# Performance work log

Measured on AMD Instinct MI355X. Metric: run time of the kernel, lower is better.

## Reference

```python
import jax, jax.numpy as jnp
import numpy as np

DIM = 384
HEADS = 8


def setup_inputs() -> dict:
    key = jax.random.key(0)
    k_x, k_qkv, k_pw, k_pb = jax.random.split(key, 4)
    x = jax.random.normal(k_x, (8, DIM, 32, 32), dtype=jnp.float32)
    # Conv2d 1x1 weights stored as [out, in]
    w_qkv = jax.random.normal(k_qkv, (3 * DIM, DIM), dtype=jnp.float32) * (DIM ** -0.5)
    w_proj = jax.random.normal(k_pw, (DIM, DIM), dtype=jnp.float32) * (DIM ** -0.5)
    b_proj = jax.random.normal(k_pb, (DIM,), dtype=jnp.float32) * 0.02
    return {"x": x, "w_qkv": w_qkv, "w_proj": w_proj, "b_proj": b_proj}


def reference(x, w_qkv, w_proj, b_proj):
    B, C, H, W = x.shape
    h = HEADS
    d = C // h
    scale = d ** -0.5
    # 1x1 conv == channel-wise linear: [B,3C,H,W]
    qkv = jnp.einsum('oc,bchw->bohw', w_qkv, x)
    q, k, v = jnp.split(qkv, 3, axis=1)
    # B (h d) H W -> B h (H W) d
    def to_heads(y):
        return y.reshape(B, h, d, H * W).transpose(0, 1, 3, 2)
    q, k, v = to_heads(q), to_heads(k), to_heads(v)
    att = jnp.einsum('bhxd,bhyd->bhxy', q * scale, k)
    att = jax.nn.softmax(att, axis=-1)
    out = jnp.einsum('bhxy,bhyd->bhxd', att, v)
    # B h (H W) d -> B (h d) H W
    out = out.transpose(0, 1, 3, 2).reshape(B, C, H, W)
    out = jnp.einsum('oc,bchw->bohw', w_proj, out) + b_proj[None, :, None, None]
    return out
```

## Files before the change

kernel.cpp:

```cpp
#include <hip/hip_runtime.h>
#include <math.h>

typedef unsigned short u16;
typedef __attribute__((ext_vector_type(8))) short short8;
typedef __attribute__((ext_vector_type(8))) unsigned short ushort8;
typedef __attribute__((ext_vector_type(4))) float floatx4;
typedef __attribute__((ext_vector_type(2))) unsigned int uint2v;

#define SEQ 1024
#define CDIM 384
#define NH 8
#define DH 48
#define DP 64
#define NB 8

__device__ __forceinline__ u16 f2bf(float f){
  unsigned int u; __builtin_memcpy(&u, &f, 4);
  u = (u + 0x7fffu + ((u >> 16) & 1u)) >> 16;
  return (u16)u;
}
__device__ __forceinline__ unsigned packbf(float a, float b){
  unsigned ua, ub; __builtin_memcpy(&ua, &a, 4); __builtin_memcpy(&ub, &b, 4);
  ua += 0x7fffu + ((ua >> 16) & 1u);
  ub += 0x7fffu + ((ub >> 16) & 1u);
  return __builtin_amdgcn_perm(ub, ua, 0x07060302);
}
__device__ __forceinline__ void async16(const u16* g, u16* l){
  __builtin_amdgcn_global_load_lds((const __attribute__((address_space(1))) void*)g,
                                   (__attribute__((address_space(3))) void*)l, 16, 0, 0);
}

__global__ __launch_bounds__(256) void prep_kernel(const float* __restrict__ x,
                                                   const float* __restrict__ wq,
                                                   const float* __restrict__ wp,
                                                   u16* __restrict__ xT,
                                                   u16* __restrict__ wdst){
  __shared__ u16 ldsT[64 * 72];
  const int id = blockIdx.x;
  const int t = threadIdx.x;
  if (id < 768){
    const int bx = id & 15, by = (id >> 4) % 6, bz = id / 96;
    const int c0 = by * 64;
    const int s0 = bx * 64;
    const int rr = t >> 2, q4 = t & 3;

    const float* src = x + ((size_t)(bz * CDIM + c0 + rr)) * SEQ + s0;
#pragma unroll
    for (int i = 0; i < 4; i++){
      const int cc = q4 + i * 4;
      float4 f = *(const float4*)(src + cc * 4);
      ldsT[(cc * 4 + 0) * 72 + rr] = f2bf(f.x);
      ldsT[(cc * 4 + 1) * 72 + rr] = f2bf(f.y);
      ldsT[(cc * 4 + 2) * 72 + rr] = f2bf(f.z);
      ldsT[(cc * 4 + 3) * 72 + rr] = f2bf(f.w);
    }
    __syncthreads();
    u16* dst = xT + ((size_t)(bz * SEQ + s0 + rr)) * CDIM + c0 + q4 * 16;
    *(ushort8*)(dst)     = *(const ushort8*)&ldsT[rr * 72 + q4 * 16];
    *(ushort8*)(dst + 8) = *(const ushort8*)&ldsT[rr * 72 + q4 * 16 + 8];
  } else {
    const int NWQ = 3 * CDIM * CDIM;
    const int i = ((id - 768) * 256 + t) * 4;
    const float* src = (i < NWQ) ? (wq + i) : (wp + (i - NWQ));
    float4 f = *(const float4*)src;
    uint2v v; v[0] = packbf(f.x, f.y); v[1] = packbf(f.z, f.w);
    *(uint2v*)(wdst + i) = v;
  }
}

__global__ __launch_bounds__(256) void qkv_kernel(const u16* __restrict__ W,
                                                  const u16* __restrict__ xT,
                                                  u16* __restrict__ qws,
                                                  u16* __restrict__ kws,
                                                  u16* __restrict__ vws){
  __shared__ u16 ldsA[128 * 64];
  __shared__ u16 ldsB[64 * 64];
  const int t = threadIdx.x;
  const int w = t >> 6, l = t & 63;
  const int quad = l >> 4, li = l & 15;
  const int n0 = blockIdx.x * 64;
  const int m0 = blockIdx.y * 128;
  const int b  = blockIdx.z;

  floatx4 acc[2][4];
#pragma unroll
  for (int i = 0; i < 2; i++)
#pragma unroll
    for (int j = 0; j < 4; j++) acc[i][j] = (floatx4)0.0f;

  const u16* xb = xT + (size_t)b * SEQ * CDIM;
  const int swz = li & 7;

  for (int kk = 0; kk < CDIM; kk += 64){
    __syncthreads();
#pragma unroll
    for (int rep = 0; rep < 4; rep++){
      const int cs = rep * 256 + t;
      const int row = cs >> 3, c4 = cs & 7;
      async16(&W[(size_t)(m0 + row) * CDIM + kk + ((c4 ^ (row & 7)) << 3)], &ldsA[cs * 8]);
    }
#pragma unroll
    for (int rep = 0; rep < 2; rep++){
      const int cs = rep * 256 + t;
      const int row = cs >> 3, c4 = cs & 7;
      async16(&xb[(size_t)(n0 + row) * CDIM + kk + ((c4 ^ (row & 7)) << 3)], &ldsB[cs * 8]);
    }
    __syncthreads();
#pragma unroll
    for (int kc = 0; kc < 2; kc++){
      const int rc = ((kc * 4 + quad) ^ swz) << 3;
      short8 af[2], bf[4];
#pragma unroll
      for (int i = 0; i < 2; i++)
        af[i] = *(const short8*)&ldsA[(w * 32 + i * 16 + li) * 64 + rc];
#pragma unroll
      for (int j = 0; j < 4; j++)
        bf[j] = *(const short8*)&ldsB[(j * 16 + li) * 64 + rc];
#pragma unroll
      for (int i = 0; i < 2; i++)
#pragma unroll
        for (int j = 0; j < 4; j++)
          acc[i][j] = __builtin_amdgcn_mfma_f32_16x16x32_bf16(af[i], bf[j], acc[i][j], 0, 0, 0);
    }
  }

  const float qs = 0.14433756729740643f * 1.4426950408889634f;
  const uint2v z2 = (uint2v)0u;
#pragma unroll
  for (int i = 0; i < 2; i++){
    const int obase = m0 + w * 32 + i * 16 + quad * 4;
    const int which = obase / CDIM;
    const int rem = obase - which * CDIM;
    const int h = rem / DH;
    const int dd = rem - h * DH;
    const int pair = b * NH + h;
#pragma unroll
    for (int j = 0; j < 4; j++){
      const int s = n0 + j * 16 + li;
      floatx4 v = acc[i][j];
      if (which == 0){
        uint2v pk; pk[0] = packbf(v[0] * qs, v[1] * qs); pk[1] = packbf(v[2] * qs, v[3] * qs);
        *(uint2v*)&qws[((size_t)pair * SEQ + s) * DP + dd] = pk;
        if ((dd & 48) == 32)
          *(uint2v*)&qws[((size_t)pair * SEQ + s) * DP + dd + 16] = z2;
      } else if (which == 1){
        uint2v pk; pk[0] = packbf(v[0], v[1]); pk[1] = packbf(v[2], v[3]);
        *(uint2v*)&kws[((size_t)pair * SEQ + s) * DP + dd] = pk;
        if ((dd & 48) == 32)
          *(uint2v*)&kws[((size_t)pair * SEQ + s) * DP + dd + 16] = z2;
      } else {
#pragma unroll
        for (int r = 0; r < 4; r++)
          vws[((size_t)pair * DH + dd + r) * SEQ + s] = f2bf(v[r]);
      }
    }
  }
}

__global__ __launch_bounds__(256) void attn_kernel(const u16* __restrict__ qws,
                                                   const u16* __restrict__ kws,
                                                   const u16* __restrict__ vws,
                                                   u16* __restrict__ aT){
  __shared__ u16 ldsK[2][64 * 64];
  __shared__ u16 ldsV[2][48 * 64];
  __shared__ u16 ldsP[64 * 72];

  const int t = threadIdx.x;
  const int w = t >> 6, l = t & 63;
  const int quad = l >> 4, li = l & 15;
  const int id = blockIdx.x;
  const int pair = id & 63;
  const int qb = id >> 6;
  const int b = pair >> 3, h = pair & 7;
  const int qbase = qb * 64 + w * 16;
  const int swz = li & 7;

  const u16* qrow = qws + ((size_t)pair * SEQ + qbase + li) * DP;
  const short8 qf0 = *(const short8*)(qrow + quad * 8);
  const short8 qf1 = *(const short8*)(qrow + 32 + quad * 8);

  floatx4 ot[3];
#pragma unroll
  for (int dt = 0; dt < 3; dt++) ot[dt] = (floatx4)0.0f;
  float m_run = -3.0e38f, l_run = 0.0f;

  const u16* kbase = kws + (size_t)pair * SEQ * DP;
  const u16* vbase = vws + (size_t)pair * DH * SEQ;

  auto stage = [&](int kv, int pp){
#pragma unroll
    for (int rep = 0; rep < 4; rep++){
      const int cs = rep * 256 + t;
      if (cs < 512){
        const int row = cs >> 3, c4 = cs & 7;
        async16(&kbase[(size_t)(kv + row) * DP + ((c4 ^ (row & 7)) << 3)],
                &ldsK[pp][cs * 8]);
      } else if (cs < 896){
        const int cs2 = cs - 512;
        const int row = cs2 >> 3, c4 = cs2 & 7;
        async16(&vbase[(size_t)row * SEQ + kv + ((c4 ^ (row & 7)) << 3)],
                &ldsV[pp][cs2 * 8]);
      }
    }
  };

  u16* prow = ldsP + (w * 16 + li) * 72;

  stage(0, 0);
  for (int i = 0; i < 16; i++){
    const int p = i & 1;
    __syncthreads();
    if (i < 15) stage((i + 1) * 64, p ^ 1);

    floatx4 st[4];
#pragma unroll
    for (int yt = 0; yt < 4; yt++){
      const u16* krow = ldsK[p] + (yt * 16 + li) * 64;
      const short8 kf0 = *(const short8*)(krow + (((0 + quad) ^ swz) << 3));
      const short8 kf1 = *(const short8*)(krow + (((4 + quad) ^ swz) << 3));
      floatx4 z = (floatx4)0.0f;
      z = __builtin_amdgcn_mfma_f32_16x16x32_bf16(kf0, qf0, z, 0, 0, 0);
      z = __builtin_amdgcn_mfma_f32_16x16x32_bf16(kf1, qf1, z, 0, 0, 0);
      st[yt] = z;
    }

    float mx = -3.0e38f;
#pragma unroll
    for (int yt = 0; yt < 4; yt++)
#pragma unroll
      for (int r = 0; r < 4; r++) mx = fmaxf(mx, st[yt][r]);
    mx = fmaxf(mx, __shfl_xor(mx, 16, 64));
    mx = fmaxf(mx, __shfl_xor(mx, 32, 64));
    const float mnew = fmaxf(m_run, mx);
    const float alpha = __builtin_amdgcn_exp2f(m_run - mnew);
    m_run = mnew;

    float ls = 0.0f;
#pragma unroll
    for (int yt = 0; yt < 4; yt++){
      float p0 = __builtin_amdgcn_exp2f(st[yt][0] - mnew);
      float p1 = __builtin_amdgcn_exp2f(st[yt][1] - mnew);
      float p2 = __builtin_amdgcn_exp2f(st[yt][2] - mnew);
      float p3 = __builtin_amdgcn_exp2f(st[yt][3] - mnew);
      ls += (p0 + p1) + (p2 + p3);
      uint2v pk; pk[0] = packbf(p0, p1); pk[1] = packbf(p2, p3);
      *(uint2v*)&prow[yt * 16 + quad * 4] = pk;
    }
    l_run = l_run * alpha + ls;
#pragma unroll
    for (int dt = 0; dt < 3; dt++) ot[dt] *= alpha;

#pragma unroll
    for (int ks = 0; ks < 64; ks += 32){
      const short8 pb = *(const short8*)&ldsP[(w * 16 + li) * 72 + ks + quad * 8];
#pragma unroll
      for (int dt = 0; dt < 3; dt++){
        const short8 vf = *(const short8*)&ldsV[p][(dt * 16 + li) * 64 +
                                                  ((((ks >> 3) + quad) ^ swz) << 3)];
        ot[dt] = __builtin_amdgcn_mfma_f32_16x16x32_bf16(vf, pb, ot[dt], 0, 0, 0);
      }
    }
  }

  float ls = l_run;
  ls += __shfl_xor(ls, 16, 64);
  ls += __shfl_xor(ls, 32, 64);
  const float rl = __builtin_amdgcn_rcpf(ls);
  const int q = qbase + li;
#pragma unroll
  for (int dt = 0; dt < 3; dt++){
    floatx4 v = ot[dt];
    uint2v pk; pk[0] = packbf(v[0] * rl, v[1] * rl); pk[1] = packbf(v[2] * rl, v[3] * rl);
    *(uint2v*)&aT[((size_t)b * SEQ + q) * CDIM + h * DH + dt * 16 + quad * 4] = pk;
  }
}

__global__ __launch_bounds__(256) void proj_kernel(const u16* __restrict__ W,
                                                   const u16* __restrict__ aT,
                                                   const float* __restrict__ bias,
                                                   float* __restrict__ out){
  __shared__ u16 ldsA[128 * 64];
  __shared__ u16 ldsB[64 * 64];
  const int t = threadIdx.x;
  const int w = t >> 6, l = t & 63;
  const int quad = l >> 4, li = l & 15;
  const int n0 = blockIdx.x * 64;
  const int m0 = blockIdx.y * 128;
  const int b  = blockIdx.z;

  floatx4 acc[2][4];
#pragma unroll
  for (int i = 0; i < 2; i++)
#pragma unroll
    for (int j = 0; j < 4; j++) acc[i][j] = (floatx4)0.0f;

  const u16* ab = aT + (size_t)b * SEQ * CDIM;
  const int swz = li & 7;

  for (int kk = 0; kk < CDIM; kk += 64){
    __syncthreads();
#pragma unroll
    for (int rep = 0; rep < 4; rep++){
      const int cs = rep * 256 + t;
      const int row = cs >> 3, c4 = cs & 7;
      async16(&W[(size_t)(m0 + row) * CDIM + kk + ((c4 ^ (row & 7)) << 3)], &ldsA[cs * 8]);
    }
#pragma unroll
    for (int rep = 0; rep < 2; rep++){
      const int cs = rep * 256 + t;
      const int row = cs >> 3, c4 = cs & 7;
      async16(&ab[(size_t)(n0 + row) * CDIM + kk + ((c4 ^ (row & 7)) << 3)], &ldsB[cs * 8]);
    }
    __syncthreads();
#pragma unroll
    for (int kc = 0; kc < 2; kc++){
      const int rc = ((kc * 4 + quad) ^ swz) << 3;
      short8 af[2], bf[4];
#pragma unroll
      for (int i = 0; i < 2; i++)
        af[i] = *(const short8*)&ldsA[(w * 32 + i * 16 + li) * 64 + rc];
#pragma unroll
      for (int j = 0; j < 4; j++)
        bf[j] = *(const short8*)&ldsB[(j * 16 + li) * 64 + rc];
#pragma unroll
      for (int i = 0; i < 2; i++)
#pragma unroll
        for (int j = 0; j < 4; j++)
          acc[i][j] = __builtin_amdgcn_mfma_f32_16x16x32_bf16(af[i], bf[j], acc[i][j], 0, 0, 0);
    }
  }

#pragma unroll
  for (int i = 0; i < 2; i++){
    const int o0 = m0 + w * 32 + i * 16 + quad * 4;
    float bs[4];
#pragma unroll
    for (int r = 0; r < 4; r++) bs[r] = bias[o0 + r];
#pragma unroll
    for (int j = 0; j < 4; j++){
      const int s = n0 + j * 16 + li;
#pragma unroll
      for (int r = 0; r < 4; r++)
        out[((size_t)b * CDIM + o0 + r) * SEQ + s] = acc[i][j][r] + bs[r];
    }
  }
}

extern "C" void kernel_launch(void* const* d_in, const int* in_sizes, int n_in,
                              void* d_out, int out_size, void* d_ws, size_t ws_size,
                              hipStream_t stream) {
  const float* x      = (const float*)d_in[0];
  const float* w_qkv  = (const float*)d_in[1];
  const float* w_proj = (const float*)d_in[2];
  const float* b_proj = (const float*)d_in[3];
  float* out = (float*)d_out;

  char* ws = (char*)d_ws;
  const size_t SZX = (size_t)NB * SEQ * CDIM * sizeof(u16);
  const size_t SZQ = (size_t)NB * NH * SEQ * DP * sizeof(u16);
  const size_t SZV = (size_t)NB * NH * SEQ * DH * sizeof(u16);
  u16* xT   = (u16*)(ws);
  u16* qws  = (u16*)(ws + SZX);
  u16* kws  = (u16*)(ws + SZX + SZQ);
  u16* vws  = (u16*)(ws + SZX + 2 * SZQ);
  u16* wq_b = (u16*)(ws + SZX + 2 * SZQ + SZV);
  u16* wp_b = wq_b + (size_t)3 * CDIM * CDIM;
  u16* aT   = xT;

  prep_kernel<<<dim3(768 + 576), 256, 0, stream>>>(x, w_qkv, w_proj, xT, wq_b);
  qkv_kernel<<<dim3(16, 9, 8), 256, 0, stream>>>(wq_b, xT, qws, kws, vws);
  attn_kernel<<<dim3(1024), 256, 0, stream>>>(qws, kws, vws, aT);
  proj_kernel<<<dim3(16, 3, 8), 256, 0, stream>>>(wp_b, aT, b_proj, out);
}
```

Measured before the change: 127.0 us.

## Fuse fp32-to-bf16 conversion and transpose into QKV and projection GEMM loaders

Removes the separate prep kernel that converted x and the weights to bf16 and transposed x into a workspace. The QKV and projection GEMMs now read fp32 directly into registers, convert to bf16 and write swizzled or padded tiles to LDS, with the next k-tile register-prefetched during compute. This saves one launch and a full bf16 round trip of x through global memory. In exchange, the weights are reconverted by every block, fp32 loads double the global read bytes, and the async LDS loads are replaced by register staging that raises register pressure.

```diff
diff --git a/kernel.cpp b/kernel.cpp
--- a/kernel.cpp
+++ b/kernel.cpp
@@ -3,9 +3,9 @@
 
 typedef unsigned short u16;
 typedef __attribute__((ext_vector_type(8))) short short8;
-typedef __attribute__((ext_vector_type(8))) unsigned short ushort8;
 typedef __attribute__((ext_vector_type(4))) float floatx4;
 typedef __attribute__((ext_vector_type(2))) unsigned int uint2v;
+typedef __attribute__((ext_vector_type(4))) unsigned int uint4v;
 
 #define SEQ 1024
 #define CDIM 384
@@ -30,51 +30,13 @@
                                    (__attribute__((address_space(3))) void*)l, 16, 0, 0);
 }
 
-__global__ __launch_bounds__(256) void prep_kernel(const float* __restrict__ x,
-                                                   const float* __restrict__ wq,
-                                                   const float* __restrict__ wp,
-                                                   u16* __restrict__ xT,
-                                                   u16* __restrict__ wdst){
-  __shared__ u16 ldsT[64 * 72];
-  const int id = blockIdx.x;
-  const int t = threadIdx.x;
-  if (id < 768){
-    const int bx = id & 15, by = (id >> 4) % 6, bz = id / 96;
-    const int c0 = by * 64;
-    const int s0 = bx * 64;
-    const int rr = t >> 2, q4 = t & 3;
-
-    const float* src = x + ((size_t)(bz * CDIM + c0 + rr)) * SEQ + s0;
-#pragma unroll
-    for (int i = 0; i < 4; i++){
-      const int cc = q4 + i * 4;
-      float4 f = *(const float4*)(src + cc * 4);
-      ldsT[(cc * 4 + 0) * 72 + rr] = f2bf(f.x);
-      ldsT[(cc * 4 + 1) * 72 + rr] = f2bf(f.y);
-      ldsT[(cc * 4 + 2) * 72 + rr] = f2bf(f.z);
-      ldsT[(cc * 4 + 3) * 72 + rr] = f2bf(f.w);
-    }
-    __syncthreads();
-    u16* dst = xT + ((size_t)(bz * SEQ + s0 + rr)) * CDIM + c0 + q4 * 16;
-    *(ushort8*)(dst)     = *(const ushort8*)&ldsT[rr * 72 + q4 * 16];
-    *(ushort8*)(dst + 8) = *(const ushort8*)&ldsT[rr * 72 + q4 * 16 + 8];
-  } else {
-    const int NWQ = 3 * CDIM * CDIM;
-    const int i = ((id - 768) * 256 + t) * 4;
-    const float* src = (i < NWQ) ? (wq + i) : (wp + (i - NWQ));
-    float4 f = *(const float4*)src;
-    uint2v v; v[0] = packbf(f.x, f.y); v[1] = packbf(f.z, f.w);
-    *(uint2v*)(wdst + i) = v;
-  }
-}
-
-__global__ __launch_bounds__(256) void qkv_kernel(const u16* __restrict__ W,
-                                                  const u16* __restrict__ xT,
+__global__ __launch_bounds__(256) void qkv_kernel(const float* __restrict__ W,
+                                                  const float* __restrict__ x,
                                                   u16* __restrict__ qws,
                                                   u16* __restrict__ kws,
                                                   u16* __restrict__ vws){
   __shared__ u16 ldsA[128 * 64];
-  __shared__ u16 ldsB[64 * 64];
+  __shared__ u16 ldsB[64 * 72];
   const int t = threadIdx.x;
   const int w = t >> 6, l = t & 63;
   const int quad = l >> 4, li = l & 15;
@@ -88,24 +50,53 @@
 #pragma unroll
     for (int j = 0; j < 4; j++) acc[i][j] = (floatx4)0.0f;
 
-  const u16* xb = xT + (size_t)b * SEQ * CDIM;
+  const float* xb = x + (size_t)b * CDIM * SEQ;
   const int swz = li & 7;
 
+  const int orow = t >> 1, ohalf = (t & 1) * 32;
+  const int cpair = t >> 3, si = t & 7;
+
+  float4 areg[8];
+  float4 b00, b01, b10, b11;
+  {
+    const float* ar = W + (size_t)(m0 + orow) * CDIM + ohalf;
+#pragma unroll
+    for (int j = 0; j < 8; j++) areg[j] = *(const float4*)(ar + j * 4);
+    const float* r0 = xb + (size_t)(cpair * 2) * SEQ + n0 + si * 8;
+    b00 = *(const float4*)r0;        b01 = *(const float4*)(r0 + 4);
+    b10 = *(const float4*)(r0+SEQ);  b11 = *(const float4*)(r0 + SEQ + 4);
+  }
+
   for (int kk = 0; kk < CDIM; kk += 64){
     __syncthreads();
 #pragma unroll
-    for (int rep = 0; rep < 4; rep++){
-      const int cs = rep * 256 + t;
-      const int row = cs >> 3, c4 = cs & 7;
-      async16(&W[(size_t)(m0 + row) * CDIM + kk + ((c4 ^ (row & 7)) << 3)], &ldsA[cs * 8]);
-    }
-#pragma unroll
-    for (int rep = 0; rep < 2; rep++){
-      const int cs = rep * 256 + t;
-      const int row = cs >> 3, c4 = cs & 7;
-      async16(&xb[(size_t)(n0 + row) * CDIM + kk + ((c4 ^ (row & 7)) << 3)], &ldsB[cs * 8]);
-    }
-    __syncthreads();
+    for (int j = 0; j < 4; j++){
+      uint4v v;
+      v[0] = packbf(areg[2*j].x,   areg[2*j].y);
+      v[1] = packbf(areg[2*j].z,   areg[2*j].w);
+      v[2] = packbf(areg[2*j+1].x, areg[2*j+1].y);
+      v[3] = packbf(areg[2*j+1].z, areg[2*j+1].w);
+      const int chunk = (((t & 1) * 4 + j) ^ (orow & 7));
+      *(uint4v*)&ldsA[orow * 64 + chunk * 8] = v;
+    }
+    {
+      const float ca[8] = {b00.x,b00.y,b00.z,b00.w, b01.x,b01.y,b01.z,b01.w};
+      const float cb[8] = {b10.x,b10.y,b10.z,b10.w, b11.x,b11.y,b11.z,b11.w};
+#pragma unroll
+      for (int j = 0; j < 8; j++)
+        *(unsigned*)&ldsB[(si * 8 + j) * 72 + cpair * 2] = packbf(ca[j], cb[j]);
+    }
+    __syncthreads();
+
+    if (kk + 64 < CDIM){
+      const float* ar = W + (size_t)(m0 + orow) * CDIM + kk + 64 + ohalf;
+#pragma unroll
+      for (int j = 0; j < 8; j++) areg[j] = *(const float4*)(ar + j * 4);
+      const float* r0 = xb + (size_t)(kk + 64 + cpair * 2) * SEQ + n0 + si * 8;
+      b00 = *(const float4*)r0;        b01 = *(const float4*)(r0 + 4);
+      b10 = *(const float4*)(r0+SEQ);  b11 = *(const float4*)(r0 + SEQ + 4);
+    }
+
 #pragma unroll
     for (int kc = 0; kc < 2; kc++){
       const int rc = ((kc * 4 + quad) ^ swz) << 3;
@@ -115,7 +106,7 @@
         af[i] = *(const short8*)&ldsA[(w * 32 + i * 16 + li) * 64 + rc];
 #pragma unroll
       for (int j = 0; j < 4; j++)
-        bf[j] = *(const short8*)&ldsB[(j * 16 + li) * 64 + rc];
+        bf[j] = *(const short8*)&ldsB[(j * 16 + li) * 72 + kc * 32 + quad * 8];
 #pragma unroll
       for (int i = 0; i < 2; i++)
 #pragma unroll
@@ -275,7 +266,7 @@
   }
 }
 
-__global__ __launch_bounds__(256) void proj_kernel(const u16* __restrict__ W,
+__global__ __launch_bounds__(256) void proj_kernel(const float* __restrict__ W,
                                                    const u16* __restrict__ aT,
                                                    const float* __restrict__ bias,
                                                    float* __restrict__ out){
@@ -296,14 +287,26 @@
 
   const u16* ab = aT + (size_t)b * SEQ * CDIM;
   const int swz = li & 7;
+  const int orow = t >> 1, ohalf = (t & 1) * 32;
+
+  float4 areg[8];
+  {
+    const float* ar = W + (size_t)(m0 + orow) * CDIM + ohalf;
+#pragma unroll
+    for (int j = 0; j < 8; j++) areg[j] = *(const float4*)(ar + j * 4);
+  }
 
   for (int kk = 0; kk < CDIM; kk += 64){
     __syncthreads();
 #pragma unroll
-    for (int rep = 0; rep < 4; rep++){
-      const int cs = rep * 256 + t;
-      const int row = cs >> 3, c4 = cs & 7;
-      async16(&W[(size_t)(m0 + row) * CDIM + kk + ((c4 ^ (row & 7)) << 3)], &ldsA[cs * 8]);
+    for (int j = 0; j < 4; j++){
+      uint4v v;
+      v[0] = packbf(areg[2*j].x,   areg[2*j].y);
+      v[1] = packbf(areg[2*j].z,   areg[2*j].w);
+      v[2] = packbf(areg[2*j+1].x, areg[2*j+1].y);
+      v[3] = packbf(areg[2*j+1].z, areg[2*j+1].w);
+      const int chunk = (((t & 1) * 4 + j) ^ (orow & 7));
+      *(uint4v*)&ldsA[orow * 64 + chunk * 8] = v;
     }
 #pragma unroll
     for (int rep = 0; rep < 2; rep++){
@@ -312,6 +315,13 @@
       async16(&ab[(size_t)(n0 + row) * CDIM + kk + ((c4 ^ (row & 7)) << 3)], &ldsB[cs * 8]);
     }
     __syncthreads();
+
+    if (kk + 64 < CDIM){
+      const float* ar = W + (size_t)(m0 + orow) * CDIM + kk + 64 + ohalf;
+#pragma unroll
+      for (int j = 0; j < 8; j++) areg[j] = *(const float4*)(ar + j * 4);
+    }
+
 #pragma unroll
     for (int kc = 0; kc < 2; kc++){
       const int rc = ((kc * 4 + quad) ^ swz) << 3;
@@ -358,17 +368,12 @@
   char* ws = (char*)d_ws;
   const size_t SZX = (size_t)NB * SEQ * CDIM * sizeof(u16);
   const size_t SZQ = (size_t)NB * NH * SEQ * DP * sizeof(u16);
-  const size_t SZV = (size_t)NB * NH * SEQ * DH * sizeof(u16);
-  u16* xT   = (u16*)(ws);
-  u16* qws  = (u16*)(ws + SZX);
-  u16* kws  = (u16*)(ws + SZX + SZQ);
-  u16* vws  = (u16*)(ws + SZX + 2 * SZQ);
-  u16* wq_b = (u16*)(ws + SZX + 2 * SZQ + SZV);
-  u16* wp_b = wq_b + (size_t)3 * CDIM * CDIM;
-  u16* aT   = xT;
-
-  prep_kernel<<<dim3(768 + 576), 256, 0, stream>>>(x, w_qkv, w_proj, xT, wq_b);
-  qkv_kernel<<<dim3(16, 9, 8), 256, 0, stream>>>(wq_b, xT, qws, kws, vws);
+  u16* aT  = (u16*)(ws);
+  u16* qws = (u16*)(ws + SZX);
+  u16* kws = (u16*)(ws + SZX + SZQ);
+  u16* vws = (u16*)(ws + SZX + 2 * SZQ);
+
+  qkv_kernel<<<dim3(16, 9, 8), 256, 0, stream>>>(w_qkv, x, qws, kws, vws);
   attn_kernel<<<dim3(1024), 256, 0, stream>>>(qws, kws, vws, aT);
-  proj_kernel<<<dim3(16, 3, 8), 256, 0, stream>>>(wp_b, aT, b_proj, out);
-}
+  proj_kernel<<<dim3(16, 3, 8), 256, 0, stream>>>(w_proj, aT, b_proj, out);
+}
```

Measured after the change: 157.7 us. 24.1% more time.
